# Performance work log

Measured on AMD Instinct MI355X. Metric: run time of the kernel, lower is better.

Reference implementation:

```python
import jax, jax.numpy as jnp
import numpy as np

B, S, D = 8, 1024, 768
H = 12
DH = D // H  # 64


def setup_inputs() -> dict:
    key = jax.random.key(0)
    ks = jax.random.split(key, 9)
    s = 0.02
    return {
        "x": jax.random.normal(ks[0], (B, S, D), dtype=jnp.float32),
        # per-head QKV projections stacked over heads: [H, D, DH]
        "Wq": jax.random.normal(ks[1], (H, D, DH), dtype=jnp.float32) * s,
        "bq": jax.random.normal(ks[2], (H, DH), dtype=jnp.float32) * s,
        "Wk": jax.random.normal(ks[3], (H, D, DH), dtype=jnp.float32) * s,
        "bk": jax.random.normal(ks[4], (H, DH), dtype=jnp.float32) * s,
        "Wv": jax.random.normal(ks[5], (H, D, DH), dtype=jnp.float32) * s,
        "bv": jax.random.normal(ks[6], (H, DH), dtype=jnp.float32) * s,
        # output projection: [D, D] (applied as x @ Wo + bo)
        "Wo": jax.random.normal(ks[7], (D, D), dtype=jnp.float32) * s,
        "bo": jax.random.normal(ks[8], (D,), dtype=jnp.float32) * s,
    }


def reference(x, Wq, bq, Wk, bk, Wv, bv, Wo, bo):
    # Per-head linear projections, vectorized over heads -> [B, H, S, DH]
    q = jnp.einsum("bsd,hde->bhse", x, Wq) + bq[None, :, None, :]
    k = jnp.einsum("bsd,hde->bhse", x, Wk) + bk[None, :, None, :]
    v = jnp.einsum("bsd,hde->bhse", x, Wv) + bv[None, :, None, :]
    scale = 1.0 / jnp.sqrt(jnp.asarray(DH, dtype=q.dtype))
    scores = jnp.einsum("bhse,bhte->bhst", q, k) * scale  # [B,H,S,S]
    probs = jax.nn.softmax(scores, axis=-1)  # dropout p=0 (eval)
    out = jnp.einsum("bhst,bhte->bhse", probs, v)  # [B,H,S,DH]
    # concat heads (head order matches ModuleList order) -> [B,S,D]
    out = out.transpose(0, 2, 1, 3).reshape(B, S, D)
    return out @ Wo + bo
```

## Files before the change

### kernel.cpp

```cpp
#include <hip/hip_runtime.h>
#include <math.h>

#define BB 8
#define SS 1024
#define DD 768
#define HH 12
#define DHH 64
#define BSS (BB*SS)
#define NQKV 2304
#define NT 24

typedef _Float16 half8 __attribute__((ext_vector_type(8)));
typedef _Float16 half4 __attribute__((ext_vector_type(4)));
typedef float    f32x4 __attribute__((ext_vector_type(4)));

__device__ __forceinline__ void glds16(const _Float16* g, _Float16* l)
{
    __builtin_amdgcn_global_load_lds(
        (const __attribute__((address_space(1))) uint32_t*)(g),
        (__attribute__((address_space(3))) uint32_t*)(l),
        16, 0, 0);
}

__global__ __launch_bounds__(256)
void prep(const float* __restrict__ x, _Float16* __restrict__ xh,
          const float* __restrict__ Wq, const float* __restrict__ Wk,
          const float* __restrict__ Wv, const float* __restrict__ Wo,
          _Float16* __restrict__ Wt, _Float16* __restrict__ Wot)
{
    const int blk = blockIdx.x;
    const int tid = threadIdx.x;

    if (blk < 3072) {
        int i = blk * 256 + tid;
        const float4* xp = (const float4*)x + (size_t)i * 2;
        float4 u = xp[0], v = xp[1];
        half8 h = { (_Float16)u.x, (_Float16)u.y, (_Float16)u.z, (_Float16)u.w,
                    (_Float16)v.x, (_Float16)v.y, (_Float16)v.z, (_Float16)v.w };
        ((half8*)xh)[i] = h;
        return;
    }

    __shared__ float T[64][65];
    const int t  = blk - 3072;
    const int z  = t / 144;
    const int r_ = t - z * 144;
    const int d0 = (r_ / 12) * 64;
    const int n_outer = r_ % 12;

    const float* src;
    _Float16* dst;
    int base_mul, row_stride;
    if (z < 3) {
        src = (z == 0) ? Wq : (z == 1) ? Wk : Wv;
        dst = Wt + (size_t)z * DD * DD;
        base_mul = DD * DHH; row_stride = DHH;
    } else {
        src = Wo; dst = Wot;
        base_mul = 64; row_stride = DD;
    }

    const size_t base = (size_t)n_outer * base_mul;
    {
        int dl = tid >> 2, c0 = (tid & 3) * 16;
        const float* p = src + base + (size_t)(d0 + dl) * row_stride + c0;
#pragma unroll
        for (int m = 0; m < 4; ++m) {
            float4 f = *(const float4*)(p + m * 4);
            T[dl][c0 + m*4 + 0] = f.x;
            T[dl][c0 + m*4 + 1] = f.y;
            T[dl][c0 + m*4 + 2] = f.z;
            T[dl][c0 + m*4 + 3] = f.w;
        }
    }
    __syncthreads();
    {
        int e = tid >> 2, c = tid & 3;
        half8 lo, hi;
#pragma unroll
        for (int i = 0; i < 8; ++i) {
            lo[i] = (_Float16)T[c*16 + i][e];
            hi[i] = (_Float16)T[c*16 + 8 + i][e];
        }
        _Float16* q = dst + ((size_t)n_outer * 64 + e) * DD + d0 + c * 16;
        *(half8*)q = lo;
        *(half8*)(q + 8) = hi;
    }
}

#define WAITV(N) asm volatile("s_waitcnt vmcnt(" #N ")" ::: "memory")

__global__ __launch_bounds__(512, 2)
void gemm_qkv_256x288(const _Float16* __restrict__ Xh, const _Float16* __restrict__ Wt,
                      const float* __restrict__ bq, const float* __restrict__ bk,
                      const float* __restrict__ bv,
                      _Float16* __restrict__ qo, _Float16* __restrict__ ko,
                      _Float16* __restrict__ vto)
{
    __shared__ _Float16 Ab[4][256][32];
    __shared__ _Float16 Bb[4][288][32];

    const int bid = blockIdx.x;
    const int c8  = bid & 7;
    const int g   = bid >> 3;
    const int m_t = c8 * 4 + (g >> 3);
    const int n_t = g & 7;
    const int m0 = m_t * 256;
    const int n0 = n_t * 288;

    const int tid  = threadIdx.x;
    const int wave = tid >> 6;
    const int lane = tid & 63;
    const int l16  = tid & 15;
    const int quad = (tid >> 4) & 3;
    const int wy = wave >> 1;
    const int wx = wave & 1;

    const int scol = ((lane & 3) ^ ((lane >> 3) & 3)) * 8;
    const int fcol = (quad ^ ((l16 >> 1) & 3)) * 8;

    const bool big = (wave == 0) || (wave == 4);

    const _Float16* apA = Xh + (size_t)(m0 + 32 * wave + (lane >> 2)) * DD + scol;
    const _Float16* bpB = Wt + (size_t)(n0 + 32 * wave + (lane >> 2)) * DD + scol;
    const _Float16* bpX = Wt + (size_t)(n0 + 256 + ((wave & 4) << 2) + (lane >> 2)) * DD + scol;
    const int xrow = 256 + ((wave & 4) << 2);

#define STAGE(buf, kt) do {                                               \
        glds16(apA + (kt) * 32,           &Ab[buf][32 * wave][0]);        \
        glds16(apA + (kt) * 32 + 16 * DD, &Ab[buf][32 * wave + 16][0]);   \
        glds16(bpB + (kt) * 32,           &Bb[buf][32 * wave][0]);        \
        glds16(bpB + (kt) * 32 + 16 * DD, &Bb[buf][32 * wave + 16][0]);   \
        if (big) glds16(bpX + (kt) * 32,  &Bb[buf][xrow][0]);             \
    } while (0)

    f32x4 acc[4][9];
#pragma unroll
    for (int i = 0; i < 4; ++i)
#pragma unroll
        for (int j = 0; j < 9; ++j) acc[i][j] = (f32x4){0.f, 0.f, 0.f, 0.f};

    STAGE(0, 0); STAGE(1, 1); STAGE(2, 2);
    if (big) WAITV(10); else WAITV(8);
    __builtin_amdgcn_s_barrier();

    for (int kt = 0; kt < NT; ++kt) {
        const int buf = kt & 3;

        half8 a[4], bf[9];
#pragma unroll
        for (int i = 0; i < 4; ++i)
            a[i] = *(const half8*)&Ab[buf][wy * 64 + i * 16 + l16][fcol];
#pragma unroll
        for (int j = 0; j < 9; ++j)
            bf[j] = *(const half8*)&Bb[buf][wx * 144 + j * 16 + l16][fcol];

        if (kt < NT - 3) {
            const int nb = (kt + 3) & 3;
            STAGE(nb, kt + 3);
        }

        __builtin_amdgcn_s_setprio(1);
#pragma unroll
        for (int i = 0; i < 4; ++i)
#pragma unroll
            for (int j = 0; j < 9; ++j)
                acc[i][j] = __builtin_amdgcn_mfma_f32_16x16x32_f16(a[i], bf[j], acc[i][j], 0, 0, 0);
        __builtin_amdgcn_s_setprio(0);

        if (kt < NT - 3) {
            if (big) WAITV(10); else WAITV(8);
            __builtin_amdgcn_s_barrier();
        } else if (kt == NT - 3) {
            if (big) WAITV(5); else WAITV(4);
            __builtin_amdgcn_s_barrier();
        } else if (kt == NT - 2) {
            WAITV(0);
            __builtin_amdgcn_s_barrier();
        }
    }
#undef STAGE

    float bvv[9]; int hh9[9], ee9[9], ws9[9];
#pragma unroll
    for (int j = 0; j < 9; ++j) {
        int nl = n0 + wx * 144 + j * 16 + l16;
        int ws = nl / 768;
        int nloc = nl - ws * 768;
        const float* bp_ = (ws == 0) ? bq : (ws == 1) ? bk : bv;
        bvv[j] = bp_[nloc];
        hh9[j] = nloc >> 6;
        ee9[j] = nloc & 63;
        ws9[j] = ws;
    }

#pragma unroll
    for (int i = 0; i < 4; ++i) {
#pragma unroll
        for (int r = 0; r < 4; ++r) {
            int row = m0 + wy * 64 + i * 16 + quad * 4 + r;
            int b_ = row >> 10;
            int s  = row & (SS - 1);
#pragma unroll
            for (int j = 0; j < 9; ++j) {
                float val = acc[i][j][r] + bvv[j];
                if (ws9[j] == 0)
                    qo[((size_t)(b_ * HH + hh9[j]) * SS + s) * DHH + ee9[j]] = (_Float16)(val * 0.125f);
                else if (ws9[j] == 1)
                    ko[((size_t)(b_ * HH + hh9[j]) * SS + s) * DHH + ee9[j]] = (_Float16)val;
                else
                    vto[((size_t)(b_ * HH + hh9[j]) * DHH + ee9[j]) * SS + s] = (_Float16)val;
            }
        }
    }
}

__global__ __launch_bounds__(256)
void gemm_out_f16(const _Float16* __restrict__ Ah, const _Float16* __restrict__ Bt,
                  const float* __restrict__ bias, float* __restrict__ out)
{
    __shared__ _Float16 Ash[2][128][32];
    __shared__ _Float16 Bsh[2][64][32];

    const int m0 = blockIdx.x * 128;
    const int n0 = blockIdx.y * 64;
    const int tid  = threadIdx.x;
    const int wave = tid >> 6;
    const int lane = tid & 63;
    const int l16  = tid & 15;
    const int quad = (tid >> 4) & 3;
    const int wy = wave >> 1;
    const int wx = wave & 1;

    const int scol = ((lane & 3) ^ ((lane >> 3) & 3)) * 8;
    const int fcol = (quad ^ ((l16 >> 1) & 3)) * 8;

    const _Float16* ap = Ah + (size_t)(m0 + 32 * wave + (lane >> 2)) * DD + scol;
    const _Float16* bp = Bt + (size_t)(n0 + 16 * wave + (lane >> 2)) * DD + scol;

    f32x4 acc[4][2];
#pragma unroll
    for (int i = 0; i < 4; ++i)
#pragma unroll
        for (int j = 0; j < 2; ++j) acc[i][j] = (f32x4){0.f, 0.f, 0.f, 0.f};

    glds16(ap, &Ash[0][32 * wave][0]);
    glds16(ap + 16 * DD, &Ash[0][32 * wave + 16][0]);
    glds16(bp, &Bsh[0][16 * wave][0]);

    int cur = 0;
    for (int k0 = 0; k0 < DD; k0 += 32) {
        __syncthreads();
        if (k0 + 32 < DD) {
            glds16(ap + k0 + 32, &Ash[cur ^ 1][32 * wave][0]);
            glds16(ap + k0 + 32 + 16 * DD, &Ash[cur ^ 1][32 * wave + 16][0]);
            glds16(bp + k0 + 32, &Bsh[cur ^ 1][16 * wave][0]);
        }

        half8 a[4], bf[2];
#pragma unroll
        for (int i = 0; i < 4; ++i)
            a[i] = *(const half8*)&Ash[cur][wy * 64 + i * 16 + l16][fcol];
#pragma unroll
        for (int j = 0; j < 2; ++j)
            bf[j] = *(const half8*)&Bsh[cur][wx * 32 + j * 16 + l16][fcol];
#pragma unroll
        for (int i = 0; i < 4; ++i)
#pragma unroll
            for (int j = 0; j < 2; ++j)
                acc[i][j] = __builtin_amdgcn_mfma_f32_16x16x32_f16(a[i], bf[j], acc[i][j], 0, 0, 0);
        cur ^= 1;
    }

#pragma unroll
    for (int i = 0; i < 4; ++i) {
#pragma unroll
        for (int r = 0; r < 4; ++r) {
            int row = m0 + wy * 64 + i * 16 + quad * 4 + r;
#pragma unroll
            for (int j = 0; j < 2; ++j) {
                int col = n0 + wx * 32 + j * 16 + l16;
                out[(size_t)row * DD + col] = acc[i][j][r] + bias[col];
            }
        }
    }
}

__global__ __launch_bounds__(512)
void attn_f16(const _Float16* __restrict__ qh, const _Float16* __restrict__ kh,
              const _Float16* __restrict__ vt, _Float16* __restrict__ ctxh)
{
    const int bh  = blockIdx.x;
    const int q0  = blockIdx.y * 128;
    const int tid = threadIdx.x;
    const int wave = tid >> 6;
    const int lane = tid & 63;
    const int l16  = tid & 15;
    const int quad = (tid >> 4) & 3;

    __shared__ _Float16 Ks[2][2][64][32];
    __shared__ _Float16 Vt[2][2][64][32];
    __shared__ _Float16 Pt[8][16][72];

    const int scol = ((lane & 3) ^ ((lane >> 3) & 3)) * 8;
    const int fcol = (quad ^ ((l16 >> 1) & 3)) * 8;

    const _Float16* qrow = qh + ((size_t)bh * SS + q0 + wave * 16 + l16) * DHH;
    const half8 qlo = *(const half8*)(qrow + quad * 8);
    const half8 qhi = *(const half8*)(qrow + 32 + quad * 8);

    const int sw = wave & 3;
    const _Float16* kp = kh + ((size_t)bh * SS + 16 * sw + (lane >> 2)) * DHH + scol;
    const _Float16* vp = vt + ((size_t)bh * DHH + 16 * sw + (lane >> 2)) * SS + scol;

    f32x4 o[4];
    float lacc = 0.f;
#pragma unroll
    for (int j = 0; j < 4; ++j) o[j] = (f32x4){0.f, 0.f, 0.f, 0.f};

    if (wave < 4) {
        glds16(kp,      &Ks[0][0][16 * sw][0]);
        glds16(kp + 32, &Ks[0][1][16 * sw][0]);
    } else {
        glds16(vp,      &Vt[0][0][16 * sw][0]);
        glds16(vp + 32, &Vt[0][1][16 * sw][0]);
    }

    int cur = 0;
    for (int kt = 0; kt < SS; kt += 64) {
        __syncthreads();
        if (kt + 64 < SS) {
            if (wave < 4) {
                glds16(kp + (size_t)(kt + 64) * DHH,      &Ks[cur ^ 1][0][16 * sw][0]);
                glds16(kp + (size_t)(kt + 64) * DHH + 32, &Ks[cur ^ 1][1][16 * sw][0]);
            } else {
                glds16(vp + kt + 64,      &Vt[cur ^ 1][0][16 * sw][0]);
                glds16(vp + kt + 64 + 32, &Vt[cur ^ 1][1][16 * sw][0]);
            }
        }

#pragma unroll
        for (int f = 0; f < 4; ++f) {
            half8 klo = *(const half8*)&Ks[cur][0][f * 16 + l16][fcol];
            half8 khi = *(const half8*)&Ks[cur][1][f * 16 + l16][fcol];
            f32x4 z = (f32x4){0.f, 0.f, 0.f, 0.f};
            z = __builtin_amdgcn_mfma_f32_16x16x32_f16(klo, qlo, z, 0, 0, 0);
            z = __builtin_amdgcn_mfma_f32_16x16x32_f16(khi, qhi, z, 0, 0, 0);
            half4 pk;
#pragma unroll
            for (int r = 0; r < 4; ++r) {
                float p = __expf(z[r]);
                lacc += p;
                pk[r] = (_Float16)p;
            }
            *(half4*)&Pt[wave][l16][f * 16 + quad * 4] = pk;
        }

        half8 pl = *(const half8*)&Pt[wave][l16][quad * 8];
        half8 ph = *(const half8*)&Pt[wave][l16][32 + quad * 8];

#pragma unroll
        for (int j = 0; j < 4; ++j) {
            half8 vlo = *(const half8*)&Vt[cur][0][j * 16 + l16][fcol];
            half8 vhi = *(const half8*)&Vt[cur][1][j * 16 + l16][fcol];
            o[j] = __builtin_amdgcn_mfma_f32_16x16x32_f16(pl, vlo, o[j], 0, 0, 0);
            o[j] = __builtin_amdgcn_mfma_f32_16x16x32_f16(ph, vhi, o[j], 0, 0, 0);
        }
        cur ^= 1;
    }

    float lr = lacc;
    lr += __shfl_xor(lr, 16);
    lr += __shfl_xor(lr, 32);

    const int b_ = bh / HH;
    const int h_ = bh % HH;
#pragma unroll
    for (int r = 0; r < 4; ++r) {
        float invl = 1.f / __shfl(lr, quad * 4 + r, 16);
        int s_ = q0 + wave * 16 + quad * 4 + r;
        _Float16* orow = ctxh + ((size_t)(b_ * SS + s_)) * DD + h_ * DHH;
#pragma unroll
        for (int j = 0; j < 4; ++j)
            orow[j * 16 + l16] = (_Float16)(o[j][r] * invl);
    }
}

extern "C" void kernel_launch(void* const* d_in, const int* in_sizes, int n_in,
                              void* d_out, int out_size, void* d_ws, size_t ws_size,
                              hipStream_t stream)
{
    const float* x  = (const float*)d_in[0];
    const float* Wq = (const float*)d_in[1];
    const float* bq = (const float*)d_in[2];
    const float* Wk = (const float*)d_in[3];
    const float* bk = (const float*)d_in[4];
    const float* Wv = (const float*)d_in[5];
    const float* bv = (const float*)d_in[6];
    const float* Wo = (const float*)d_in[7];
    const float* bo = (const float*)d_in[8];
    float* out = (float*)d_out;

    const size_t xe = (size_t)BSS * DD;
    const size_t we = (size_t)DD * DD;
    _Float16* Xh   = (_Float16*)d_ws;
    _Float16* Wt   = Xh  + xe;
    _Float16* Wot  = Wt  + (size_t)3 * we;
    _Float16* qhb  = Wot + we;
    _Float16* khb  = qhb + xe;
    _Float16* vtb  = khb + xe;
    _Float16* ctxh = vtb + xe;

    prep<<<3072 + 576, 256, 0, stream>>>(x, Xh, Wq, Wk, Wv, Wo, Wt, Wot);

    gemm_qkv_256x288<<<(BSS / 256) * (NQKV / 288), 512, 0, stream>>>(
        Xh, Wt, bq, bk, bv, qhb, khb, vtb);

    dim3 ag(BB * HH, SS / 128);
    attn_f16<<<ag, 512, 0, stream>>>(qhb, khb, vtb, ctxh);

    dim3 gg(BSS / 128, DD / 64);
    gemm_out_f16<<<gg, 256, 0, stream>>>(ctxh, Wot, bo, out);
}
```

Baseline: 212.2 us.

## Retile QKV GEMM to 256x128 and triple-buffer both projection GEMMs

```diff
diff --git a/kernel.cpp b/kernel.cpp
--- a/kernel.cpp
+++ b/kernel.cpp
@@ -21,6 +21,8 @@
         (__attribute__((address_space(3))) uint32_t*)(l),
         16, 0, 0);
 }
+
+#define WAITV(N) asm volatile("s_waitcnt vmcnt(" #N ")" ::: "memory")
 
 __global__ __launch_bounds__(256)
 void prep(const float* __restrict__ x, _Float16* __restrict__ xh,
@@ -88,25 +90,23 @@
     }
 }
 
-#define WAITV(N) asm volatile("s_waitcnt vmcnt(" #N ")" ::: "memory")
-
-__global__ __launch_bounds__(512, 2)
-void gemm_qkv_256x288(const _Float16* __restrict__ Xh, const _Float16* __restrict__ Wt,
+__global__ __launch_bounds__(256, 2)
+void gemm_qkv_256x128(const _Float16* __restrict__ Xh, const _Float16* __restrict__ Wt,
                       const float* __restrict__ bq, const float* __restrict__ bk,
                       const float* __restrict__ bv,
                       _Float16* __restrict__ qo, _Float16* __restrict__ ko,
                       _Float16* __restrict__ vto)
 {
-    __shared__ _Float16 Ab[4][256][32];
-    __shared__ _Float16 Bb[4][288][32];
+    __shared__ _Float16 Ab[3][256][32];
+    __shared__ _Float16 Bb[3][128][32];
 
     const int bid = blockIdx.x;
     const int c8  = bid & 7;
     const int g   = bid >> 3;
-    const int m_t = c8 * 4 + (g >> 3);
-    const int n_t = g & 7;
+    const int m_t = c8 * 4 + g / 18;
+    const int n_t = g % 18;
     const int m0 = m_t * 256;
-    const int n0 = n_t * 288;
+    const int n0 = n_t * 128;
 
     const int tid  = threadIdx.x;
     const int wave = tid >> 6;
@@ -119,99 +119,118 @@
     const int scol = ((lane & 3) ^ ((lane >> 3) & 3)) * 8;
     const int fcol = (quad ^ ((l16 >> 1) & 3)) * 8;
 
-    const bool big = (wave == 0) || (wave == 4);
-
-    const _Float16* apA = Xh + (size_t)(m0 + 32 * wave + (lane >> 2)) * DD + scol;
+    const _Float16* apA = Xh + (size_t)(m0 + 64 * wave + (lane >> 2)) * DD + scol;
     const _Float16* bpB = Wt + (size_t)(n0 + 32 * wave + (lane >> 2)) * DD + scol;
-    const _Float16* bpX = Wt + (size_t)(n0 + 256 + ((wave & 4) << 2) + (lane >> 2)) * DD + scol;
-    const int xrow = 256 + ((wave & 4) << 2);
 
 #define STAGE(buf, kt) do {                                               \
-        glds16(apA + (kt) * 32,           &Ab[buf][32 * wave][0]);        \
-        glds16(apA + (kt) * 32 + 16 * DD, &Ab[buf][32 * wave + 16][0]);   \
+        glds16(apA + (kt) * 32,           &Ab[buf][64 * wave][0]);        \
+        glds16(apA + (kt) * 32 + 16 * DD, &Ab[buf][64 * wave + 16][0]);   \
+        glds16(apA + (kt) * 32 + 32 * DD, &Ab[buf][64 * wave + 32][0]);   \
+        glds16(apA + (kt) * 32 + 48 * DD, &Ab[buf][64 * wave + 48][0]);   \
         glds16(bpB + (kt) * 32,           &Bb[buf][32 * wave][0]);        \
         glds16(bpB + (kt) * 32 + 16 * DD, &Bb[buf][32 * wave + 16][0]);   \
-        if (big) glds16(bpX + (kt) * 32,  &Bb[buf][xrow][0]);             \
     } while (0)
 
-    f32x4 acc[4][9];
-#pragma unroll
-    for (int i = 0; i < 4; ++i)
-#pragma unroll
-        for (int j = 0; j < 9; ++j) acc[i][j] = (f32x4){0.f, 0.f, 0.f, 0.f};
-
-    STAGE(0, 0); STAGE(1, 1); STAGE(2, 2);
-    if (big) WAITV(10); else WAITV(8);
+    f32x4 acc[8][4];
+#pragma unroll
+    for (int i = 0; i < 8; ++i)
+#pragma unroll
+        for (int j = 0; j < 4; ++j) acc[i][j] = (f32x4){0.f, 0.f, 0.f, 0.f};
+
+#define QCOMPUTE(buf)                                                       \
+    {                                                                       \
+        half8 a[8], bf[4];                                                  \
+        _Pragma("unroll")                                                   \
+        for (int i = 0; i < 8; ++i)                                         \
+            a[i] = *(const half8*)&Ab[buf][wy * 128 + i * 16 + l16][fcol];  \
+        _Pragma("unroll")                                                   \
+        for (int j = 0; j < 4; ++j)                                         \
+            bf[j] = *(const half8*)&Bb[buf][wx * 64 + j * 16 + l16][fcol];  \
+        __builtin_amdgcn_s_setprio(1);                                      \
+        _Pragma("unroll")                                                   \
+        for (int i = 0; i < 8; ++i)                                         \
+            _Pragma("unroll")                                               \
+            for (int j = 0; j < 4; ++j)                                     \
+                acc[i][j] = __builtin_amdgcn_mfma_f32_16x16x32_f16(a[i], bf[j], acc[i][j], 0, 0, 0); \
+        __builtin_amdgcn_s_setprio(0);                                      \
+    }
+
+    STAGE(0, 0); STAGE(1, 1);
+    WAITV(6);
     __builtin_amdgcn_s_barrier();
 
-    for (int kt = 0; kt < NT; ++kt) {
-        const int buf = kt & 3;
-
-        half8 a[4], bf[9];
-#pragma unroll
-        for (int i = 0; i < 4; ++i)
-            a[i] = *(const half8*)&Ab[buf][wy * 64 + i * 16 + l16][fcol];
-#pragma unroll
-        for (int j = 0; j < 9; ++j)
-            bf[j] = *(const half8*)&Bb[buf][wx * 144 + j * 16 + l16][fcol];
-
-        if (kt < NT - 3) {
-            const int nb = (kt + 3) & 3;
-            STAGE(nb, kt + 3);
-        }
-
-        __builtin_amdgcn_s_setprio(1);
-#pragma unroll
-        for (int i = 0; i < 4; ++i)
-#pragma unroll
-            for (int j = 0; j < 9; ++j)
-                acc[i][j] = __builtin_amdgcn_mfma_f32_16x16x32_f16(a[i], bf[j], acc[i][j], 0, 0, 0);
-        __builtin_amdgcn_s_setprio(0);
-
-        if (kt < NT - 3) {
-            if (big) WAITV(10); else WAITV(8);
-            __builtin_amdgcn_s_barrier();
-        } else if (kt == NT - 3) {
-            if (big) WAITV(5); else WAITV(4);
-            __builtin_amdgcn_s_barrier();
-        } else if (kt == NT - 2) {
-            WAITV(0);
-            __builtin_amdgcn_s_barrier();
-        }
-    }
+    int cur = 0;
+    for (int kt = 0; kt < NT - 2; ++kt) {
+        const int stg = cur ? cur - 1 : 2;
+        STAGE(stg, kt + 2);
+        QCOMPUTE(cur);
+        WAITV(6);
+        __builtin_amdgcn_s_barrier();
+        cur = (cur == 2) ? 0 : cur + 1;
+    }
+    QCOMPUTE(1);
+    WAITV(0);
+    __builtin_amdgcn_s_barrier();
+    QCOMPUTE(2);
+
+#undef QCOMPUTE
 #undef STAGE
 
-    float bvv[9]; int hh9[9], ee9[9], ws9[9];
-#pragma unroll
-    for (int j = 0; j < 9; ++j) {
-        int nl = n0 + wx * 144 + j * 16 + l16;
-        int ws = nl / 768;
-        int nloc = nl - ws * 768;
-        const float* bp_ = (ws == 0) ? bq : (ws == 1) ? bk : bv;
-        bvv[j] = bp_[nloc];
-        hh9[j] = nloc >> 6;
-        ee9[j] = nloc & 63;
-        ws9[j] = ws;
-    }
-
-#pragma unroll
-    for (int i = 0; i < 4; ++i) {
-#pragma unroll
-        for (int r = 0; r < 4; ++r) {
-            int row = m0 + wy * 64 + i * 16 + quad * 4 + r;
-            int b_ = row >> 10;
-            int s  = row & (SS - 1);
-#pragma unroll
-            for (int j = 0; j < 9; ++j) {
-                float val = acc[i][j][r] + bvv[j];
-                if (ws9[j] == 0)
-                    qo[((size_t)(b_ * HH + hh9[j]) * SS + s) * DHH + ee9[j]] = (_Float16)(val * 0.125f);
-                else if (ws9[j] == 1)
-                    ko[((size_t)(b_ * HH + hh9[j]) * SS + s) * DHH + ee9[j]] = (_Float16)val;
-                else
-                    vto[((size_t)(b_ * HH + hh9[j]) * DHH + ee9[j]) * SS + s] = (_Float16)val;
-            }
-        }
+    const int wsel = n0 / 768;
+    const int nb = n0 - wsel * 768 + wx * 64;
+    const float* bp_ = (wsel == 0) ? bq : (wsel == 1) ? bk : bv;
+
+    float bvv[4]; int hh4[4], ee4[4];
+#pragma unroll
+    for (int j = 0; j < 4; ++j) {
+        int nl = nb + j * 16 + l16;
+        bvv[j] = bp_[nl];
+        hh4[j] = nl >> 6;
+        ee4[j] = nl & 63;
+    }
+
+    if (wsel == 0) {
+#pragma unroll
+        for (int i = 0; i < 8; ++i)
+#pragma unroll
+            for (int r = 0; r < 4; ++r) {
+                int row = m0 + wy * 128 + i * 16 + quad * 4 + r;
+                int b_ = row >> 10;
+                int s  = row & (SS - 1);
+#pragma unroll
+                for (int j = 0; j < 4; ++j) {
+                    float val = (acc[i][j][r] + bvv[j]) * 0.125f;
+                    qo[((size_t)(b_ * HH + hh4[j]) * SS + s) * DHH + ee4[j]] = (_Float16)val;
+                }
+            }
+    } else if (wsel == 1) {
+#pragma unroll
+        for (int i = 0; i < 8; ++i)
+#pragma unroll
+            for (int r = 0; r < 4; ++r) {
+                int row = m0 + wy * 128 + i * 16 + quad * 4 + r;
+                int b_ = row >> 10;
+                int s  = row & (SS - 1);
+#pragma unroll
+                for (int j = 0; j < 4; ++j) {
+                    float val = acc[i][j][r] + bvv[j];
+                    ko[((size_t)(b_ * HH + hh4[j]) * SS + s) * DHH + ee4[j]] = (_Float16)val;
+                }
+            }
+    } else {
+#pragma unroll
+        for (int i = 0; i < 8; ++i)
+#pragma unroll
+            for (int r = 0; r < 4; ++r) {
+                int row = m0 + wy * 128 + i * 16 + quad * 4 + r;
+                int b_ = row >> 10;
+                int s  = row & (SS - 1);
+#pragma unroll
+                for (int j = 0; j < 4; ++j) {
+                    float val = acc[i][j][r] + bvv[j];
+                    vto[((size_t)(b_ * HH + hh4[j]) * DHH + ee4[j]) * SS + s] = (_Float16)val;
+                }
+            }
     }
 }
 
@@ -219,8 +238,8 @@
 void gemm_out_f16(const _Float16* __restrict__ Ah, const _Float16* __restrict__ Bt,
                   const float* __restrict__ bias, float* __restrict__ out)
 {
-    __shared__ _Float16 Ash[2][128][32];
-    __shared__ _Float16 Bsh[2][64][32];
+    __shared__ _Float16 Ash[3][128][32];
+    __shared__ _Float16 Bsh[3][64][32];
 
     const int m0 = blockIdx.x * 128;
     const int n0 = blockIdx.y * 64;
@@ -238,39 +257,56 @@
     const _Float16* ap = Ah + (size_t)(m0 + 32 * wave + (lane >> 2)) * DD + scol;
     const _Float16* bp = Bt + (size_t)(n0 + 16 * wave + (lane >> 2)) * DD + scol;
 
+#define OSTAGE(buf, kt) do {                                              \
+        glds16(ap + (kt) * 32,           &Ash[buf][32 * wave][0]);        \
+        glds16(ap + (kt) * 32 + 16 * DD, &Ash[buf][32 * wave + 16][0]);   \
+        glds16(bp + (kt) * 32,           &Bsh[buf][16 * wave][0]);        \
+    } while (0)
+
     f32x4 acc[4][2];
 #pragma unroll
     for (int i = 0; i < 4; ++i)
 #pragma unroll
         for (int j = 0; j < 2; ++j) acc[i][j] = (f32x4){0.f, 0.f, 0.f, 0.f};
 
-    glds16(ap, &Ash[0][32 * wave][0]);
-    glds16(ap + 16 * DD, &Ash[0][32 * wave + 16][0]);
-    glds16(bp, &Bsh[0][16 * wave][0]);
+#define OCOMPUTE(buf)                                                       \
+    {                                                                       \
+        half8 a[4], bf[2];                                                  \
+        _Pragma("unroll")                                                   \
+        for (int i = 0; i < 4; ++i)                                         \
+            a[i] = *(const half8*)&Ash[buf][wy * 64 + i * 16 + l16][fcol];  \
+        _Pragma("unroll")                                                   \
+        for (int j = 0; j < 2; ++j)                                         \
+            bf[j] = *(const half8*)&Bsh[buf][wx * 32 + j * 16 + l16][fcol]; \
+        __builtin_amdgcn_s_setprio(1);                                      \
+        _Pragma("unroll")                                                   \
+        for (int i = 0; i < 4; ++i)                                         \
+            _Pragma("unroll")                                               \
+            for (int j = 0; j < 2; ++j)                                     \
+                acc[i][j] = __builtin_amdgcn_mfma_f32_16x16x32_f16(a[i], bf[j], acc[i][j], 0, 0, 0); \
+        __builtin_amdgcn_s_setprio(0);                                      \
+    }
+
+    OSTAGE(0, 0); OSTAGE(1, 1);
+    WAITV(3);
+    __builtin_amdgcn_s_barrier();
 
     int cur = 0;
-    for (int k0 = 0; k0 < DD; k0 += 32) {
-        __syncthreads();
-        if (k0 + 32 < DD) {
-            glds16(ap + k0 + 32, &Ash[cur ^ 1][32 * wave][0]);
-            glds16(ap + k0 + 32 + 16 * DD, &Ash[cur ^ 1][32 * wave + 16][0]);
-            glds16(bp + k0 + 32, &Bsh[cur ^ 1][16 * wave][0]);
-        }
-
-        half8 a[4], bf[2];
-#pragma unroll
-        for (int i = 0; i < 4; ++i)
-            a[i] = *(const half8*)&Ash[cur][wy * 64 + i * 16 + l16][fcol];
-#pragma unroll
-        for (int j = 0; j < 2; ++j)
-            bf[j] = *(const half8*)&Bsh[cur][wx * 32 + j * 16 + l16][fcol];
-#pragma unroll
-        for (int i = 0; i < 4; ++i)
-#pragma unroll
-            for (int j = 0; j < 2; ++j)
-                acc[i][j] = __builtin_amdgcn_mfma_f32_16x16x32_f16(a[i], bf[j], acc[i][j], 0, 0, 0);
-        cur ^= 1;
-    }
+    for (int kt = 0; kt < NT - 2; ++kt) {
+        const int stg = cur ? cur - 1 : 2;
+        OSTAGE(stg, kt + 2);
+        OCOMPUTE(cur);
+        WAITV(3);
+        __builtin_amdgcn_s_barrier();
+        cur = (cur == 2) ? 0 : cur + 1;
+    }
+    OCOMPUTE(1);
+    WAITV(0);
+    __builtin_amdgcn_s_barrier();
+    OCOMPUTE(2);
+
+#undef OCOMPUTE
+#undef OSTAGE
 
 #pragma unroll
     for (int i = 0; i < 4; ++i) {
@@ -413,7 +449,7 @@
 
     prep<<<3072 + 576, 256, 0, stream>>>(x, Xh, Wq, Wk, Wv, Wo, Wt, Wot);
 
-    gemm_qkv_256x288<<<(BSS / 256) * (NQKV / 288), 512, 0, stream>>>(
+    gemm_qkv_256x128<<<(BSS / 256) * (NQKV / 128), 256, 0, stream>>>(
         Xh, Wt, bq, bk, bv, qhb, khb, vtb);
 
     dim3 ag(BB * HH, SS / 128);
```

Measured after the change: 207.2 us. -2.4%, faster.

## Split QKV GEMM tile compute into halves and triple-buffer output GEMM

Applied to the files above, without the earlier changes.

```diff
diff --git a/kernel.cpp b/kernel.cpp
--- a/kernel.cpp
+++ b/kernel.cpp
@@ -21,6 +21,8 @@
         (__attribute__((address_space(3))) uint32_t*)(l),
         16, 0, 0);
 }
+
+#define WAITV(N) asm volatile("s_waitcnt vmcnt(" #N ")" ::: "memory")
 
 __global__ __launch_bounds__(256)
 void prep(const float* __restrict__ x, _Float16* __restrict__ xh,
@@ -88,14 +90,12 @@
     }
 }
 
-#define WAITV(N) asm volatile("s_waitcnt vmcnt(" #N ")" ::: "memory")
-
 __global__ __launch_bounds__(512, 2)
-void gemm_qkv_256x288(const _Float16* __restrict__ Xh, const _Float16* __restrict__ Wt,
-                      const float* __restrict__ bq, const float* __restrict__ bk,
-                      const float* __restrict__ bv,
-                      _Float16* __restrict__ qo, _Float16* __restrict__ ko,
-                      _Float16* __restrict__ vto)
+void gemm_qkv_v5(const _Float16* __restrict__ Xh, const _Float16* __restrict__ Wt,
+                 const float* __restrict__ bq, const float* __restrict__ bk,
+                 const float* __restrict__ bv,
+                 _Float16* __restrict__ qo, _Float16* __restrict__ ko,
+                 _Float16* __restrict__ vto)
 {
     __shared__ _Float16 Ab[4][256][32];
     __shared__ _Float16 Bb[4][288][32];
@@ -126,9 +126,11 @@
     const _Float16* bpX = Wt + (size_t)(n0 + 256 + ((wave & 4) << 2) + (lane >> 2)) * DD + scol;
     const int xrow = 256 + ((wave & 4) << 2);
 
-#define STAGE(buf, kt) do {                                               \
+#define STAGE_A(buf, kt) do {                                             \
         glds16(apA + (kt) * 32,           &Ab[buf][32 * wave][0]);        \
         glds16(apA + (kt) * 32 + 16 * DD, &Ab[buf][32 * wave + 16][0]);   \
+    } while (0)
+#define STAGE_B(buf, kt) do {                                             \
         glds16(bpB + (kt) * 32,           &Bb[buf][32 * wave][0]);        \
         glds16(bpB + (kt) * 32 + 16 * DD, &Bb[buf][32 * wave + 16][0]);   \
         if (big) glds16(bpX + (kt) * 32,  &Bb[buf][xrow][0]);             \
@@ -140,46 +142,65 @@
 #pragma unroll
         for (int j = 0; j < 9; ++j) acc[i][j] = (f32x4){0.f, 0.f, 0.f, 0.f};
 
-    STAGE(0, 0); STAGE(1, 1); STAGE(2, 2);
-    if (big) WAITV(10); else WAITV(8);
+#define QTILE(buf, SA, SB)                                                  \
+    {                                                                       \
+        half8 a[4], bf[9];                                                  \
+        _Pragma("unroll")                                                   \
+        for (int i = 0; i < 4; ++i)                                         \
+            a[i] = *(const half8*)&Ab[buf][wy * 64 + i * 16 + l16][fcol];   \
+        _Pragma("unroll")                                                   \
+        for (int j = 0; j < 4; ++j)                                         \
+            bf[j] = *(const half8*)&Bb[buf][wx * 144 + j * 16 + l16][fcol]; \
+        SA;                                                                 \
+        __builtin_amdgcn_s_setprio(1);                                      \
+        _Pragma("unroll")                                                   \
+        for (int i = 0; i < 4; ++i)                                         \
+            _Pragma("unroll")                                               \
+            for (int j = 0; j < 4; ++j)                                     \
+                acc[i][j] = __builtin_amdgcn_mfma_f32_16x16x32_f16(a[i], bf[j], acc[i][j], 0, 0, 0); \
+        __builtin_amdgcn_s_setprio(0);                                      \
+        _Pragma("unroll")                                                   \
+        for (int j = 4; j < 9; ++j)                                         \
+            bf[j] = *(const half8*)&Bb[buf][wx * 144 + j * 16 + l16][fcol]; \
+        SB;                                                                 \
+        __builtin_amdgcn_s_setprio(1);                                      \
+        _Pragma("unroll")                                                   \
+        for (int i = 0; i < 4; ++i)                                         \
+            _Pragma("unroll")                                               \
+            for (int j = 4; j < 9; ++j)                                     \
+                acc[i][j] = __builtin_amdgcn_mfma_f32_16x16x32_f16(a[i], bf[j], acc[i][j], 0, 0, 0); \
+        __builtin_amdgcn_s_setprio(0);                                      \
+    }
+
+#define GATE_MAIN do { if (big) WAITV(10); else WAITV(8);                   \
+                       __builtin_amdgcn_s_barrier(); } while (0)
+
+    STAGE_A(0, 0); STAGE_B(0, 0);
+    STAGE_A(1, 1); STAGE_B(1, 1);
+    STAGE_A(2, 2); STAGE_B(2, 2);
+    GATE_MAIN;
+
+#pragma unroll 4
+    for (int kt = 0; kt < 20; ++kt) {
+        const int buf = kt & 3;
+        const int nb  = (kt + 3) & 3;
+        QTILE(buf, STAGE_A(nb, kt + 3), STAGE_B(nb, kt + 3));
+        GATE_MAIN;
+    }
+    QTILE(0, STAGE_A(3, 23), STAGE_B(3, 23));
+    GATE_MAIN;
+    QTILE(1, , );
+    if (big) WAITV(5); else WAITV(4);
     __builtin_amdgcn_s_barrier();
-
-    for (int kt = 0; kt < NT; ++kt) {
-        const int buf = kt & 3;
-
-        half8 a[4], bf[9];
-#pragma unroll
-        for (int i = 0; i < 4; ++i)
-            a[i] = *(const half8*)&Ab[buf][wy * 64 + i * 16 + l16][fcol];
-#pragma unroll
-        for (int j = 0; j < 9; ++j)
-            bf[j] = *(const half8*)&Bb[buf][wx * 144 + j * 16 + l16][fcol];
-
-        if (kt < NT - 3) {
-            const int nb = (kt + 3) & 3;
-            STAGE(nb, kt + 3);
-        }
-
-        __builtin_amdgcn_s_setprio(1);
-#pragma unroll
-        for (int i = 0; i < 4; ++i)
-#pragma unroll
-            for (int j = 0; j < 9; ++j)
-                acc[i][j] = __builtin_amdgcn_mfma_f32_16x16x32_f16(a[i], bf[j], acc[i][j], 0, 0, 0);
-        __builtin_amdgcn_s_setprio(0);
-
-        if (kt < NT - 3) {
-            if (big) WAITV(10); else WAITV(8);
-            __builtin_amdgcn_s_barrier();
-        } else if (kt == NT - 3) {
-            if (big) WAITV(5); else WAITV(4);
-            __builtin_amdgcn_s_barrier();
-        } else if (kt == NT - 2) {
-            WAITV(0);
-            __builtin_amdgcn_s_barrier();
-        }
-    }
-#undef STAGE
+    QTILE(2, , );
+    WAITV(0);
+    __builtin_amdgcn_s_barrier();
+    QTILE(3, , );
+
+#undef QTILE
+#undef GATE_MAIN
+#undef STAGE_A
+#undef STAGE_B
 
     float bvv[9]; int hh9[9], ee9[9], ws9[9];
 #pragma unroll
@@ -219,8 +240,8 @@
 void gemm_out_f16(const _Float16* __restrict__ Ah, const _Float16* __restrict__ Bt,
                   const float* __restrict__ bias, float* __restrict__ out)
 {
-    __shared__ _Float16 Ash[2][128][32];
-    __shared__ _Float16 Bsh[2][64][32];
+    __shared__ _Float16 Ash[3][128][32];
+    __shared__ _Float16 Bsh[3][64][32];
 
     const int m0 = blockIdx.x * 128;
     const int n0 = blockIdx.y * 64;
@@ -238,39 +259,56 @@
     const _Float16* ap = Ah + (size_t)(m0 + 32 * wave + (lane >> 2)) * DD + scol;
     const _Float16* bp = Bt + (size_t)(n0 + 16 * wave + (lane >> 2)) * DD + scol;
 
+#define OSTAGE(buf, kt) do {                                              \
+        glds16(ap + (kt) * 32,           &Ash[buf][32 * wave][0]);        \
+        glds16(ap + (kt) * 32 + 16 * DD, &Ash[buf][32 * wave + 16][0]);   \
+        glds16(bp + (kt) * 32,           &Bsh[buf][16 * wave][0]);        \
+    } while (0)
+
     f32x4 acc[4][2];
 #pragma unroll
     for (int i = 0; i < 4; ++i)
 #pragma unroll
         for (int j = 0; j < 2; ++j) acc[i][j] = (f32x4){0.f, 0.f, 0.f, 0.f};
 
-    glds16(ap, &Ash[0][32 * wave][0]);
-    glds16(ap + 16 * DD, &Ash[0][32 * wave + 16][0]);
-    glds16(bp, &Bsh[0][16 * wave][0]);
+#define OCOMPUTE(buf)                                                       \
+    {                                                                       \
+        half8 a[4], bf[2];                                                  \
+        _Pragma("unroll")                                                   \
+        for (int i = 0; i < 4; ++i)                                         \
+            a[i] = *(const half8*)&Ash[buf][wy * 64 + i * 16 + l16][fcol];  \
+        _Pragma("unroll")                                                   \
+        for (int j = 0; j < 2; ++j)                                         \
+            bf[j] = *(const half8*)&Bsh[buf][wx * 32 + j * 16 + l16][fcol]; \
+        __builtin_amdgcn_s_setprio(1);                                      \
+        _Pragma("unroll")                                                   \
+        for (int i = 0; i < 4; ++i)                                         \
+            _Pragma("unroll")                                               \
+            for (int j = 0; j < 2; ++j)                                     \
+                acc[i][j] = __builtin_amdgcn_mfma_f32_16x16x32_f16(a[i], bf[j], acc[i][j], 0, 0, 0); \
+        __builtin_amdgcn_s_setprio(0);                                      \
+    }
+
+    OSTAGE(0, 0); OSTAGE(1, 1);
+    WAITV(3);
+    __builtin_amdgcn_s_barrier();
 
     int cur = 0;
-    for (int k0 = 0; k0 < DD; k0 += 32) {
-        __syncthreads();
-        if (k0 + 32 < DD) {
-            glds16(ap + k0 + 32, &Ash[cur ^ 1][32 * wave][0]);
-            glds16(ap + k0 + 32 + 16 * DD, &Ash[cur ^ 1][32 * wave + 16][0]);
-            glds16(bp + k0 + 32, &Bsh[cur ^ 1][16 * wave][0]);
-        }
-
-        half8 a[4], bf[2];
-#pragma unroll
-        for (int i = 0; i < 4; ++i)
-            a[i] = *(const half8*)&Ash[cur][wy * 64 + i * 16 + l16][fcol];
-#pragma unroll
-        for (int j = 0; j < 2; ++j)
-            bf[j] = *(const half8*)&Bsh[cur][wx * 32 + j * 16 + l16][fcol];
-#pragma unroll
-        for (int i = 0; i < 4; ++i)
-#pragma unroll
-            for (int j = 0; j < 2; ++j)
-                acc[i][j] = __builtin_amdgcn_mfma_f32_16x16x32_f16(a[i], bf[j], acc[i][j], 0, 0, 0);
-        cur ^= 1;
-    }
+    for (int kt = 0; kt < NT - 2; ++kt) {
+        const int stg = cur ? cur - 1 : 2;
+        OSTAGE(stg, kt + 2);
+        OCOMPUTE(cur);
+        WAITV(3);
+        __builtin_amdgcn_s_barrier();
+        cur = (cur == 2) ? 0 : cur + 1;
+    }
+    OCOMPUTE(1);
+    WAITV(0);
+    __builtin_amdgcn_s_barrier();
+    OCOMPUTE(2);
+
+#undef OCOMPUTE
+#undef OSTAGE
 
 #pragma unroll
     for (int i = 0; i < 4; ++i) {
@@ -413,7 +451,7 @@
 
     prep<<<3072 + 576, 256, 0, stream>>>(x, Xh, Wq, Wk, Wv, Wo, Wt, Wot);
 
-    gemm_qkv_256x288<<<(BSS / 256) * (NQKV / 288), 512, 0, stream>>>(
+    gemm_qkv_v5<<<(BSS / 256) * (NQKV / 288), 512, 0, stream>>>(
         Xh, Wt, bq, bk, bv, qhb, khb, vtb);
 
     dim3 ag(BB * HH, SS / 128);
```

After: 210.3 us. No clear change (-0.9%).
